# Kernel tuning notes

Hardware: AMD Instinct MI355X
Metric: run time of the kernel (lower is better)

Reference implementation:

```python
import jax, jax.numpy as jnp
import numpy as np

B, S, DIM = 4, 2048, 512
HEADS, DHEAD = 8, 64
INNER = HEADS * DHEAD


def setup_inputs() -> dict:
    key = jax.random.key(0)
    k1, k2, k3, k4 = jax.random.split(key, 4)
    x = jax.random.normal(k1, (B, S, DIM), dtype=jnp.float32)
    W_qkv = jax.random.normal(k2, (DIM, 3 * INNER), dtype=jnp.float32) * (DIM ** -0.5)
    W_out = jax.random.normal(k3, (INNER, DIM), dtype=jnp.float32) * (INNER ** -0.5)
    b_out = jnp.zeros((DIM,), dtype=jnp.float32)
    # learnable log-temperature, initialized to log(dim_head**-0.5)
    log_temp = jnp.asarray(np.log(DHEAD ** -0.5), dtype=jnp.float32)
    return {"x": x, "W_qkv": W_qkv, "log_temp": log_temp, "W_out": W_out, "b_out": b_out}


def reference(x, W_qkv, log_temp, W_out, b_out):
    b, s, _ = x.shape
    qkv = x @ W_qkv  # [b, s, 3*inner]
    q, k, v = jnp.split(qkv, 3, axis=-1)
    # [b, s, inner] -> [b, h, s, d]
    reshape = lambda t: t.reshape(b, s, HEADS, DHEAD).transpose(0, 2, 1, 3)
    q, k, v = reshape(q), reshape(k), reshape(v)
    dots = jnp.einsum("bhid,bhjd->bhij", q, k) * jnp.exp(log_temp)
    mask_value = -jnp.finfo(dots.dtype).max
    eye = jnp.eye(s, dtype=bool)
    dots = jnp.where(eye, mask_value, dots)
    attn = jax.nn.softmax(dots, axis=-1)
    out = jnp.einsum("bhij,bhjd->bhid", attn, v)
    out = out.transpose(0, 2, 1, 3).reshape(b, s, INNER)
    return out @ W_out + b_out
```

## Files before the change

### kernel.cpp

```cpp
#include <hip/hip_runtime.h>
#include <hip/hip_bf16.h>

#define BB 4
#define SS 2048
#define DIMM 512
#define HH 8
#define DD 64
#define NQKV 1536

typedef float  floatx4 __attribute__((ext_vector_type(4)));
typedef short  bf16x8  __attribute__((ext_vector_type(8)));
typedef short  bf16x4  __attribute__((ext_vector_type(4)));

#define MFMA16(A, B, C) __builtin_amdgcn_mfma_f32_16x16x32_bf16(A, B, C, 0, 0, 0)

__device__ __forceinline__ floatx4 MFMA16K16(bf16x4 a, bf16x4 b, floatx4 c) {
#if __has_builtin(__builtin_amdgcn_mfma_f32_16x16x16bf16_1k)
    return __builtin_amdgcn_mfma_f32_16x16x16bf16_1k(a, b, c, 0, 0, 0);
#else
    floatx4 d;
    asm volatile("v_mfma_f32_16x16x16_bf16 %0, %1, %2, %3"
                 : "=v"(d) : "v"(a), "v"(b), "v"(c));
    return d;
#endif
}

__device__ __forceinline__ unsigned short f2bf(float f) {
    unsigned int u = __float_as_uint(f);
    u += 0x7FFFu + ((u >> 16) & 1u);
    return (unsigned short)(u >> 16);
}

__device__ __forceinline__ unsigned int f2bf_pk(float lo, float hi) {
    float2 f; f.x = lo; f.y = hi;
    __hip_bfloat162 h = __float22bfloat162_rn(f);
    return *reinterpret_cast<unsigned int*>(&h);
}

__device__ __forceinline__ float fast_exp2(float x) {
#if __has_builtin(__builtin_amdgcn_exp2f)
    return __builtin_amdgcn_exp2f(x);
#else
    return __exp2f(x);
#endif
}

__device__ __forceinline__ void gl_lds16(const void* g, void* l) {
    __builtin_amdgcn_global_load_lds(
        (__attribute__((address_space(1))) void*)g,
        (__attribute__((address_space(3))) void*)l,
        16, 0, 0);
}

__global__ __launch_bounds__(256) void k_prep(
    const float* __restrict__ x, const float* __restrict__ W_qkv,
    const float* __restrict__ W_out,
    unsigned short* __restrict__ xb, unsigned short* __restrict__ Wq_t,
    unsigned short* __restrict__ Wo_t) {
    __shared__ float t[32][33];
    int bid = blockIdx.x, tid = threadIdx.x;
    if (bid < 4096) {
        int i = (bid * 256 + tid) * 4;
        float4 v = *(const float4*)(x + i);
        ushort4 o;
        o.x = f2bf(v.x); o.y = f2bf(v.y); o.z = f2bf(v.z); o.w = f2bf(v.w);
        *(ushort4*)(xb + i) = o;
        return;
    }
    const float* in; unsigned short* out; int R = 512, C, bx, by;
    if (bid < 4864) { in = W_qkv; out = Wq_t; C = 1536; int blk = bid - 4096; bx = blk % 48; by = blk / 48; }
    else            { in = W_out; out = Wo_t; C = 512;  int blk = bid - 4864; bx = blk % 16; by = blk / 16; }
    int tx = tid & 31, ty = tid >> 5;
    int c0 = bx * 32, r0 = by * 32;
    for (int i = 0; i < 4; i++) {
        int r = r0 + ty + i * 8;
        t[ty + i * 8][tx] = in[(size_t)r * C + c0 + tx];
    }
    __syncthreads();
    for (int i = 0; i < 4; i++) {
        int cc = c0 + ty + i * 8;
        out[(size_t)cc * R + r0 + tx] = f2bf(t[tx][ty + i * 8]);
    }
}

__global__ __launch_bounds__(256) void k_gemm_qkv(
    const unsigned short* __restrict__ A,
    const unsigned short* __restrict__ Bt,
    const float* __restrict__ log_temp,
    unsigned short* __restrict__ Qb,
    unsigned short* __restrict__ Kb,
    unsigned short* __restrict__ Vt) {
    __shared__ unsigned short smem[2][128 * 64];
    unsigned short* As = smem[0];
    unsigned short* Bs = smem[1];
    const int K = 512;
    int m0 = blockIdx.x * 128, n0 = blockIdx.y * 128;
    int tid = threadIdx.x;
    int w = tid >> 6, lane = tid & 63;
    int c = lane & 15, q4 = lane >> 4;
    int wm = w >> 1, wn = w & 1;
    float qscale = __expf(log_temp[0]) * 1.44269504f;

    floatx4 acc[4][4] = {};

    for (int k0 = 0; k0 < K; k0 += 64) {
        __syncthreads();
        for (int i = 0; i < 4; i++) {
            int cidx = w * 256 + i * 64 + lane;
            int row = cidx >> 3, cc = cidx & 7;
            int gcc = cc ^ (row & 7);
            gl_lds16(A + (size_t)(m0 + row) * K + k0 + gcc * 8,
                     As + (size_t)(w * 256 + i * 64) * 8);
            gl_lds16(Bt + (size_t)(n0 + row) * K + k0 + gcc * 8,
                     Bs + (size_t)(w * 256 + i * 64) * 8);
        }
        __syncthreads();
        bf16x8 aF[2][4], bF[2][4];
        for (int kh = 0; kh < 2; kh++)
            for (int mt = 0; mt < 4; mt++) {
                int row = wm * 64 + mt * 16 + c;
                aF[kh][mt] = *(const bf16x8*)&As[row * 64 + (((kh * 4 + q4) ^ (row & 7)) * 8)];
            }
        for (int kh = 0; kh < 2; kh++)
            for (int nt = 0; nt < 4; nt++) {
                int row = wn * 64 + nt * 16 + c;
                bF[kh][nt] = *(const bf16x8*)&Bs[row * 64 + (((kh * 4 + q4) ^ (row & 7)) * 8)];
            }
        for (int kh = 0; kh < 2; kh++)
            for (int mt = 0; mt < 4; mt++)
                for (int nt = 0; nt < 4; nt++)
                    acc[mt][nt] = MFMA16(aF[kh][mt], bF[kh][nt], acc[mt][nt]);
    }

    if (n0 < 1024) {
        for (int nt = 0; nt < 4; nt++) {
            int n = n0 + wn * 64 + nt * 16 + c;
            int t = n >> 9, inner = n & 511;
            int h = inner >> 6, d = inner & 63;
            for (int mt = 0; mt < 4; mt++) {
                for (int r = 0; r < 4; r++) {
                    int m = m0 + wm * 64 + mt * 16 + q4 * 4 + r;
                    int b = m >> 11, s = m & 2047;
                    int bh = b * 8 + h;
                    float v = acc[mt][nt][r];
                    if (t == 0)  Qb[((size_t)bh * SS + s) * 64 + d] = f2bf(v * qscale);
                    else         Kb[((size_t)bh * SS + s) * 64 + d] = f2bf(v);
                }
            }
        }
    } else {
        unsigned short* T = &smem[0][0];
        int b = m0 >> 11, s_base = m0 & 2047;
        for (int half = 0; half < 2; half++) {
            __syncthreads();
            if (wn == half) {
                for (int nt = 0; nt < 4; nt++)
                    for (int mt = 0; mt < 4; mt++)
                        for (int r = 0; r < 4; r++)
                            T[(nt * 16 + c) * 136 + wm * 64 + mt * 16 + q4 * 4 + r] =
                                f2bf(acc[mt][nt][r]);
            }
            __syncthreads();
            for (int rr = 0; rr < 4; rr++) {
                int nl = w * 16 + rr * 4 + q4;
                int ml = c * 8;
                bf16x8 v = *(const bf16x8*)&T[nl * 136 + ml];
                int n = n0 + half * 64 + nl;
                int h = (n >> 6) - 16, d = n & 63;
                int bh = b * 8 + h;
                *(bf16x8*)(Vt + ((size_t)bh * 64 + d) * SS + s_base + ml) = v;
            }
        }
    }
}

__global__ __launch_bounds__(512, 2) void k_attn(
    const unsigned short* __restrict__ Qb,
    const unsigned short* __restrict__ Kb,
    const unsigned short* __restrict__ Vt,
    unsigned short* __restrict__ AO) {
    __shared__ unsigned short Ks[2][64 * 64];
    __shared__ unsigned short Vs[2][64 * 64];
    int q0 = blockIdx.x * 256;
    int h = blockIdx.y, b = blockIdx.z;
    int bh = b * 8 + h;
    int tid = threadIdx.x, w = tid >> 6, lane = tid & 63;
    int c = lane & 15, q4 = lane >> 4;

    const unsigned short* Kbase = Kb + (size_t)bh * SS * 64;
    const unsigned short* Vbase = Vt + (size_t)bh * 64 * SS;

    bf16x8 qf[2][2];
    for (int mi = 0; mi < 2; mi++) {
        const unsigned short* qp = Qb + ((size_t)bh * SS + q0 + w * 32 + mi * 16 + c) * 64;
        qf[mi][0] = *(const bf16x8*)(qp + q4 * 8);
        qf[mi][1] = *(const bf16x8*)(qp + 32 + q4 * 8);
    }

    int grow = tid >> 3, gcc = (tid & 7) ^ (grow & 7);
    const unsigned short* ksrc = Kbase + (size_t)grow * 64 + gcc * 8;
    const unsigned short* vsrc = Vbase + (size_t)grow * SS + gcc * 8;
    unsigned short* kdst = (unsigned short*)Ks[0] + w * 512;
    unsigned short* vdst = (unsigned short*)Vs[0] + w * 512;

    gl_lds16(ksrc, kdst);
    gl_lds16(vsrc, vdst);

    int koff0 = (q4 ^ (c & 7)) * 8;
    int koff1 = ((4 + q4) ^ (c & 7)) * 8;
    int vsub = (q4 & 1) * 4;
    int vchunk0 = (q4 >> 1);

    int mask_j0 = (q0 + w * 32) & ~63;
    int mglob0 = q0 + w * 32 + c;
    int mglob1 = mglob0 + 16;
    floatx4 oacc[2][4] = {};
    float psum0 = 0.f, psum1 = 0.f;

    for (int j0 = 0; j0 < SS; j0 += 64) {
        int buf = (j0 >> 6) & 1;
        __syncthreads();
        if (j0 + 64 < SS) {
            gl_lds16(ksrc + (size_t)(j0 + 64) * 64, kdst + (buf ^ 1) * 4096);
            gl_lds16(vsrc + (j0 + 64), vdst + (buf ^ 1) * 4096);
        }
        bool diag = (j0 == mask_j0);
        const unsigned short* KsB = Ks[buf];
        const unsigned short* VsB = Vs[buf];

#pragma unroll
        for (int jt = 0; jt < 4; jt++) {
            int rowoff = (jt * 16 + c) * 64;
            bf16x8 kf0 = *(const bf16x8*)&KsB[rowoff + koff0];
            bf16x8 kf1 = *(const bf16x8*)&KsB[rowoff + koff1];
            floatx4 sa0 = {}, sa1 = {};
            sa0 = MFMA16(kf0, qf[0][0], sa0);
            sa0 = MFMA16(kf1, qf[0][1], sa0);
            sa1 = MFMA16(kf0, qf[1][0], sa1);
            sa1 = MFMA16(kf1, qf[1][1], sa1);

            if (diag) {
#pragma unroll
                for (int r = 0; r < 4; r++) {
                    int jg = j0 + jt * 16 + q4 * 4 + r;
                    if (jg == mglob0) sa0[r] = -1e30f;
                    if (jg == mglob1) sa1[r] = -1e30f;
                }
            }

            float e0 = fast_exp2(sa0[0]), e1 = fast_exp2(sa0[1]);
            float e2 = fast_exp2(sa0[2]), e3 = fast_exp2(sa0[3]);
            psum0 += (e0 + e1) + (e2 + e3);
            union { bf16x4 v; unsigned int u[2]; } P0;
            P0.u[0] = f2bf_pk(e0, e1); P0.u[1] = f2bf_pk(e2, e3);
            float f0 = fast_exp2(sa1[0]), f1 = fast_exp2(sa1[1]);
            float f2v = fast_exp2(sa1[2]), f3 = fast_exp2(sa1[3]);
            psum1 += (f0 + f1) + (f2v + f3);
            union { bf16x4 v; unsigned int u[2]; } P1;
            P1.u[0] = f2bf_pk(f0, f1); P1.u[1] = f2bf_pk(f2v, f3);

            int chunk = jt * 2 + vchunk0;
#pragma unroll
            for (int dt = 0; dt < 4; dt++) {
                int vrow = dt * 16 + c;
                bf16x4 vf = *(const bf16x4*)&VsB[vrow * 64 + ((chunk ^ (c & 7)) * 8) + vsub];
                oacc[0][dt] = MFMA16K16(P0.v, vf, oacc[0][dt]);
                oacc[1][dt] = MFMA16K16(P1.v, vf, oacc[1][dt]);
            }
        }
    }

    for (int mi = 0; mi < 2; mi++) {
        float l = (mi == 0) ? psum0 : psum1;
        l += __shfl_xor(l, 16);
        l += __shfl_xor(l, 32);
        for (int r = 0; r < 4; r++) {
            float lr = __shfl(l, q4 * 4 + r, 64);
            float inv = 1.0f / lr;
            int s = q0 + w * 32 + mi * 16 + q4 * 4 + r;
            for (int dt = 0; dt < 4; dt++)
                AO[((size_t)b * SS + s) * 512 + h * 64 + dt * 16 + c] =
                    f2bf(oacc[mi][dt][r] * inv);
        }
    }
}

__global__ __launch_bounds__(256) void k_gemm_out(
    const unsigned short* __restrict__ A,
    const unsigned short* __restrict__ Bt,
    const float* __restrict__ bias,
    float* __restrict__ out) {
    __shared__ unsigned short As[64 * 64];
    __shared__ unsigned short Bs[128 * 64];
    const int K = 512;
    int m0 = blockIdx.x * 64, n0 = blockIdx.y * 128;
    int tid = threadIdx.x;
    int w = tid >> 6, lane = tid & 63;
    int c = lane & 15, q4 = lane >> 4;

    floatx4 acc[8] = {};

    for (int k0 = 0; k0 < K; k0 += 64) {
        __syncthreads();
        for (int i = 0; i < 2; i++) {
            int cidx = i * 256 + tid;
            int row = cidx >> 3, cc = cidx & 7;
            int gcc = cc ^ (row & 7);
            gl_lds16(A + (size_t)(m0 + row) * K + k0 + gcc * 8,
                     As + (size_t)(i * 256 + w * 64) * 8);
        }
        for (int i = 0; i < 4; i++) {
            int cidx = i * 256 + tid;
            int row = cidx >> 3, cc = cidx & 7;
            int gcc = cc ^ (row & 7);
            gl_lds16(Bt + (size_t)(n0 + row) * K + k0 + gcc * 8,
                     Bs + (size_t)(i * 256 + w * 64) * 8);
        }
        __syncthreads();
        bf16x8 aF[2], bF[2][8];
        for (int kh = 0; kh < 2; kh++) {
            int row = w * 16 + c;
            aF[kh] = *(const bf16x8*)&As[row * 64 + (((kh * 4 + q4) ^ (row & 7)) * 8)];
        }
        for (int kh = 0; kh < 2; kh++)
            for (int nt = 0; nt < 8; nt++) {
                int row = nt * 16 + c;
                bF[kh][nt] = *(const bf16x8*)&Bs[row * 64 + (((kh * 4 + q4) ^ (row & 7)) * 8)];
            }
        for (int kh = 0; kh < 2; kh++)
            for (int nt = 0; nt < 8; nt++)
                acc[nt] = MFMA16(aF[kh], bF[kh][nt], acc[nt]);
    }

    for (int nt = 0; nt < 8; nt++) {
        int n = n0 + nt * 16 + c;
        float bv = bias[n];
        for (int r = 0; r < 4; r++) {
            int m = m0 + w * 16 + q4 * 4 + r;
            out[(size_t)m * 512 + n] = acc[nt][r] + bv;
        }
    }
}

extern "C" void kernel_launch(void* const* d_in, const int* in_sizes, int n_in,
                              void* d_out, int out_size, void* d_ws, size_t ws_size,
                              hipStream_t stream) {
    const float* x        = (const float*)d_in[0];
    const float* W_qkv    = (const float*)d_in[1];
    const float* log_temp = (const float*)d_in[2];
    const float* W_out    = (const float*)d_in[3];
    const float* b_out    = (const float*)d_in[4];
    float* out = (float*)d_out;

    char* ws = (char*)d_ws;
    unsigned short* xb   = (unsigned short*)(ws + 0);
    unsigned short* Wq_t = (unsigned short*)(ws + 8388608);
    unsigned short* Wo_t = (unsigned short*)(ws + 9961472);
    unsigned short* Qb   = (unsigned short*)(ws + 10485760);
    unsigned short* Kb   = (unsigned short*)(ws + 18874368);
    unsigned short* Vt   = (unsigned short*)(ws + 27262976);
    unsigned short* AO   = (unsigned short*)(ws + 35651584);

    k_prep<<<5120, 256, 0, stream>>>(x, W_qkv, W_out, xb, Wq_t, Wo_t);
    k_gemm_qkv<<<dim3(64, 12), 256, 0, stream>>>(xb, Wq_t, log_temp, Qb, Kb, Vt);
    k_attn<<<dim3(8, 8, 4), 512, 0, stream>>>(Qb, Kb, Vt, AO);
    k_gemm_out<<<dim3(128, 4), 256, 0, stream>>>(AO, Wo_t, b_out, out);
}
```

Baseline: 168.2 us.

## Triple-buffer K/V tiles in attention and halve block size to 256 threads

The attention kernel now uses 256-thread blocks covering 128 queries each, launching twice as many blocks. K/V tiles are triple-buffered and prefetched two tiles ahead, and the per-iteration __syncthreads is replaced by an explicit vmcnt wait plus s_barrier. The aim is to hide global-to-LDS latency behind the MFMA work and to raise occupancy and block count. In exchange each thread issues more loads, LDS use grows by half, and correctness now depends on the hand-counted vmcnt value.

```diff
diff --git a/kernel.cpp b/kernel.cpp
--- a/kernel.cpp
+++ b/kernel.cpp
@@ -174,14 +174,14 @@
     }
 }
 
-__global__ __launch_bounds__(512, 2) void k_attn(
+__global__ __launch_bounds__(256, 2) void k_attn(
     const unsigned short* __restrict__ Qb,
     const unsigned short* __restrict__ Kb,
     const unsigned short* __restrict__ Vt,
     unsigned short* __restrict__ AO) {
-    __shared__ unsigned short Ks[2][64 * 64];
-    __shared__ unsigned short Vs[2][64 * 64];
-    int q0 = blockIdx.x * 256;
+    __shared__ unsigned short Ks[3][64 * 64];
+    __shared__ unsigned short Vs[3][64 * 64];
+    int q0 = blockIdx.x * 128;
     int h = blockIdx.y, b = blockIdx.z;
     int bh = b * 8 + h;
     int tid = threadIdx.x, w = tid >> 6, lane = tid & 63;
@@ -197,14 +197,25 @@
         qf[mi][1] = *(const bf16x8*)(qp + 32 + q4 * 8);
     }
 
-    int grow = tid >> 3, gcc = (tid & 7) ^ (grow & 7);
-    const unsigned short* ksrc = Kbase + (size_t)grow * 64 + gcc * 8;
-    const unsigned short* vsrc = Vbase + (size_t)grow * SS + gcc * 8;
-    unsigned short* kdst = (unsigned short*)Ks[0] + w * 512;
-    unsigned short* vdst = (unsigned short*)Vs[0] + w * 512;
-
-    gl_lds16(ksrc, kdst);
-    gl_lds16(vsrc, vdst);
+    const unsigned short* ksrc[2];
+    const unsigned short* vsrc[2];
+    int ldst[2];
+    for (int i = 0; i < 2; i++) {
+        int cidx = i * 256 + tid;
+        int grow = cidx >> 3, gcc = (cidx & 7) ^ (grow & 7);
+        ksrc[i] = Kbase + (size_t)grow * 64 + gcc * 8;
+        vsrc[i] = Vbase + (size_t)grow * SS + gcc * 8;
+        ldst[i] = (i * 256 + w * 64) * 8;
+    }
+
+    for (int i = 0; i < 2; i++) {
+        gl_lds16(ksrc[i], &Ks[0][ldst[i]]);
+        gl_lds16(vsrc[i], &Vs[0][ldst[i]]);
+    }
+    for (int i = 0; i < 2; i++) {
+        gl_lds16(ksrc[i] + (size_t)64 * 64, &Ks[1][ldst[i]]);
+        gl_lds16(vsrc[i] + 64, &Vs[1][ldst[i]]);
+    }
 
     int koff0 = (q4 ^ (c & 7)) * 8;
     int koff1 = ((4 + q4) ^ (c & 7)) * 8;
@@ -217,13 +228,24 @@
     floatx4 oacc[2][4] = {};
     float psum0 = 0.f, psum1 = 0.f;
 
+    int buf = 0;
     for (int j0 = 0; j0 < SS; j0 += 64) {
-        int buf = (j0 >> 6) & 1;
-        __syncthreads();
         if (j0 + 64 < SS) {
-            gl_lds16(ksrc + (size_t)(j0 + 64) * 64, kdst + (buf ^ 1) * 4096);
-            gl_lds16(vsrc + (j0 + 64), vdst + (buf ^ 1) * 4096);
-        }
+            asm volatile("s_waitcnt vmcnt(4)" ::: "memory");
+        } else {
+            asm volatile("s_waitcnt vmcnt(0)" ::: "memory");
+        }
+        asm volatile("s_barrier" ::: "memory");
+
+        int jn = j0 + 128;
+        if (jn < SS) {
+            int bufn = buf + 2; if (bufn >= 3) bufn -= 3;
+            for (int i = 0; i < 2; i++) {
+                gl_lds16(ksrc[i] + (size_t)jn * 64, &Ks[bufn][ldst[i]]);
+                gl_lds16(vsrc[i] + jn, &Vs[bufn][ldst[i]]);
+            }
+        }
+
         bool diag = (j0 == mask_j0);
         const unsigned short* KsB = Ks[buf];
         const unsigned short* VsB = Vs[buf];
@@ -268,6 +290,7 @@
                 oacc[1][dt] = MFMA16K16(P1.v, vf, oacc[1][dt]);
             }
         }
+        buf = buf + 1; if (buf >= 3) buf = 0;
     }
 
     for (int mi = 0; mi < 2; mi++) {
@@ -363,6 +386,6 @@
 
     k_prep<<<5120, 256, 0, stream>>>(x, W_qkv, W_out, xb, Wq_t, Wo_t);
     k_gemm_qkv<<<dim3(64, 12), 256, 0, stream>>>(xb, Wq_t, log_temp, Qb, Kb, Vt);
-    k_attn<<<dim3(8, 8, 4), 512, 0, stream>>>(Qb, Kb, Vt, AO);
+    k_attn<<<dim3(16, 8, 4), 256, 0, stream>>>(Qb, Kb, Vt, AO);
     k_gemm_out<<<dim3(128, 4), 256, 0, stream>>>(AO, Wo_t, b_out, out);
 }
```

New measurement: 168.5 us. About the same (+0.2%).

## Stage 512-key K/V tiles in LDS and coalesce Q/K/V projection stores

Applied to the files above, without the earlier changes.

The QKV projection epilogue now writes Q and K through an LDS transpose buffer, giving vectorized coalesced row stores instead of scattered scalar stores. V^T is stored with a permuted column order so the attention kernel can load 8-element V fragments in one wide LDS read. The attention kernel drops the per-64-key double buffer and loads 512-key K/V chunks into a much larger LDS buffer, with one sync pair per chunk, and launch bounds change to one block per CU. This trades fewer barriers and wider LDS reads for lower occupancy and no overlap between loads and compute.

```diff
diff --git a/kernel.cpp b/kernel.cpp
--- a/kernel.cpp
+++ b/kernel.cpp
@@ -132,25 +132,34 @@
                     acc[mt][nt] = MFMA16(aF[kh][mt], bF[kh][nt], acc[mt][nt]);
     }
 
+    int b = m0 >> 11, s_base = m0 & 2047;
     if (n0 < 1024) {
-        for (int nt = 0; nt < 4; nt++) {
-            int n = n0 + wn * 64 + nt * 16 + c;
-            int t = n >> 9, inner = n & 511;
-            int h = inner >> 6, d = inner & 63;
-            for (int mt = 0; mt < 4; mt++) {
-                for (int r = 0; r < 4; r++) {
-                    int m = m0 + wm * 64 + mt * 16 + q4 * 4 + r;
-                    int b = m >> 11, s = m & 2047;
-                    int bh = b * 8 + h;
-                    float v = acc[mt][nt][r];
-                    if (t == 0)  Qb[((size_t)bh * SS + s) * 64 + d] = f2bf(v * qscale);
-                    else         Kb[((size_t)bh * SS + s) * 64 + d] = f2bf(v);
-                }
+        bool isQ = (n0 < 512);
+        float scale = isQ ? qscale : 1.0f;
+        unsigned short* dst = isQ ? Qb : Kb;
+        unsigned short* T = &smem[0][0];
+        for (int half = 0; half < 2; half++) {
+            __syncthreads();
+            if (wn == half) {
+                for (int nt = 0; nt < 4; nt++)
+                    for (int mt = 0; mt < 4; mt++)
+                        for (int r = 0; r < 4; r++)
+                            T[(wm * 64 + mt * 16 + q4 * 4 + r) * 72 + nt * 16 + c] =
+                                f2bf(acc[mt][nt][r] * scale);
+            }
+            __syncthreads();
+            int n_base = n0 + half * 64;
+            int hq = (n_base >> 6) & 7;
+            int bh = b * 8 + hq;
+            int gg = tid & 7;
+            for (int rr = 0; rr < 4; rr++) {
+                int m = (tid >> 3) + 32 * rr;
+                bf16x8 v = *(const bf16x8*)&T[m * 72 + gg * 8];
+                *(bf16x8*)(dst + ((size_t)bh * SS + s_base + m) * 64 + gg * 8) = v;
             }
         }
     } else {
         unsigned short* T = &smem[0][0];
-        int b = m0 >> 11, s_base = m0 & 2047;
         for (int half = 0; half < 2; half++) {
             __syncthreads();
             if (wn == half) {
@@ -168,19 +177,25 @@
                 int n = n0 + half * 64 + nl;
                 int h = (n >> 6) - 16, d = n & 63;
                 int bh = b * 8 + h;
-                *(bf16x8*)(Vt + ((size_t)bh * 64 + d) * SS + s_base + ml) = v;
-            }
-        }
-    }
-}
-
-__global__ __launch_bounds__(512, 2) void k_attn(
+                int wlo = ml >> 6, a = ml & 63;
+                int j1 = wlo * 64 + (((a >> 2) & 3) << 4) + ((a >> 4) << 2);
+                unsigned short* dp = Vt + ((size_t)bh * 64 + d) * SS + s_base + j1;
+                bf16x4 lo, hi;
+                for (int i = 0; i < 4; i++) { lo[i] = v[i]; hi[i] = v[4 + i]; }
+                *(bf16x4*)dp = lo;
+                *(bf16x4*)(dp + 16) = hi;
+            }
+        }
+    }
+}
+
+__global__ __launch_bounds__(512, 1) void k_attn(
     const unsigned short* __restrict__ Qb,
     const unsigned short* __restrict__ Kb,
     const unsigned short* __restrict__ Vt,
     unsigned short* __restrict__ AO) {
-    __shared__ unsigned short Ks[2][64 * 64];
-    __shared__ unsigned short Vs[2][64 * 64];
+    __shared__ unsigned short Ks[512 * 64];
+    __shared__ unsigned short Vs[64 * 512];
     int q0 = blockIdx.x * 256;
     int h = blockIdx.y, b = blockIdx.z;
     int bh = b * 8 + h;
@@ -197,19 +212,17 @@
         qf[mi][1] = *(const bf16x8*)(qp + 32 + q4 * 8);
     }
 
-    int grow = tid >> 3, gcc = (tid & 7) ^ (grow & 7);
-    const unsigned short* ksrc = Kbase + (size_t)grow * 64 + gcc * 8;
-    const unsigned short* vsrc = Vbase + (size_t)grow * SS + gcc * 8;
-    unsigned short* kdst = (unsigned short*)Ks[0] + w * 512;
-    unsigned short* vdst = (unsigned short*)Vs[0] + w * 512;
-
-    gl_lds16(ksrc, kdst);
-    gl_lds16(vsrc, vdst);
+    int r0 = tid >> 3;
+    const unsigned short* kstage = Kbase + (size_t)r0 * 64 + (((tid & 7) ^ (r0 & 7)) * 8);
+    const unsigned short* vstage = Vbase + (size_t)w * SS + (((tid >> 3) & 7) * 64)
+                                   + (((tid & 7) ^ w) * 8);
+    unsigned short* kdst = Ks + tid * 8;
+    unsigned short* vdst = Vs + tid * 8;
 
     int koff0 = (q4 ^ (c & 7)) * 8;
     int koff1 = ((4 + q4) ^ (c & 7)) * 8;
-    int vsub = (q4 & 1) * 4;
-    int vchunk0 = (q4 >> 1);
+    int voffA = ((2 * q4) ^ (c & 7)) * 8;
+    int voffB = ((2 * q4 + 1) ^ (c & 7)) * 8;
 
     int mask_j0 = (q0 + w * 32) & ~63;
     int mglob0 = q0 + w * 32 + c;
@@ -217,55 +230,70 @@
     floatx4 oacc[2][4] = {};
     float psum0 = 0.f, psum1 = 0.f;
 
-    for (int j0 = 0; j0 < SS; j0 += 64) {
-        int buf = (j0 >> 6) & 1;
-        __syncthreads();
-        if (j0 + 64 < SS) {
-            gl_lds16(ksrc + (size_t)(j0 + 64) * 64, kdst + (buf ^ 1) * 4096);
-            gl_lds16(vsrc + (j0 + 64), vdst + (buf ^ 1) * 4096);
-        }
-        bool diag = (j0 == mask_j0);
-        const unsigned short* KsB = Ks[buf];
-        const unsigned short* VsB = Vs[buf];
-
-#pragma unroll
-        for (int jt = 0; jt < 4; jt++) {
-            int rowoff = (jt * 16 + c) * 64;
-            bf16x8 kf0 = *(const bf16x8*)&KsB[rowoff + koff0];
-            bf16x8 kf1 = *(const bf16x8*)&KsB[rowoff + koff1];
-            floatx4 sa0 = {}, sa1 = {};
-            sa0 = MFMA16(kf0, qf[0][0], sa0);
-            sa0 = MFMA16(kf1, qf[0][1], sa0);
-            sa1 = MFMA16(kf0, qf[1][0], sa1);
-            sa1 = MFMA16(kf1, qf[1][1], sa1);
-
-            if (diag) {
-#pragma unroll
-                for (int r = 0; r < 4; r++) {
-                    int jg = j0 + jt * 16 + q4 * 4 + r;
-                    if (jg == mglob0) sa0[r] = -1e30f;
-                    if (jg == mglob1) sa1[r] = -1e30f;
-                }
-            }
-
-            float e0 = fast_exp2(sa0[0]), e1 = fast_exp2(sa0[1]);
-            float e2 = fast_exp2(sa0[2]), e3 = fast_exp2(sa0[3]);
-            psum0 += (e0 + e1) + (e2 + e3);
-            union { bf16x4 v; unsigned int u[2]; } P0;
-            P0.u[0] = f2bf_pk(e0, e1); P0.u[1] = f2bf_pk(e2, e3);
-            float f0 = fast_exp2(sa1[0]), f1 = fast_exp2(sa1[1]);
-            float f2v = fast_exp2(sa1[2]), f3 = fast_exp2(sa1[3]);
-            psum1 += (f0 + f1) + (f2v + f3);
-            union { bf16x4 v; unsigned int u[2]; } P1;
-            P1.u[0] = f2bf_pk(f0, f1); P1.u[1] = f2bf_pk(f2v, f3);
-
-            int chunk = jt * 2 + vchunk0;
+    for (int mg = 0; mg < 4; mg++) {
+        int js = mg * 512;
+        __syncthreads();
+#pragma unroll
+        for (int t = 0; t < 8; t++) {
+            gl_lds16(kstage + (size_t)(js + t * 64) * 64, kdst + t * 4096);
+            gl_lds16(vstage + js + (size_t)t * 8 * SS, vdst + t * 4096);
+        }
+        __syncthreads();
+
+        for (int sub = 0; sub < 8; sub++) {
+            int j0 = js + sub * 64;
+            const unsigned short* KsB = Ks + (sub * 64) * 64;
+            const unsigned short* VsB = Vs + sub * 64;
+            bool diag = (j0 == mask_j0);
+
+            bf16x8 vA[4], vB[4];
 #pragma unroll
             for (int dt = 0; dt < 4; dt++) {
                 int vrow = dt * 16 + c;
-                bf16x4 vf = *(const bf16x4*)&VsB[vrow * 64 + ((chunk ^ (c & 7)) * 8) + vsub];
-                oacc[0][dt] = MFMA16K16(P0.v, vf, oacc[0][dt]);
-                oacc[1][dt] = MFMA16K16(P1.v, vf, oacc[1][dt]);
+                vA[dt] = *(const bf16x8*)&VsB[vrow * 512 + voffA];
+                vB[dt] = *(const bf16x8*)&VsB[vrow * 512 + voffB];
+            }
+
+#pragma unroll
+            for (int jt = 0; jt < 4; jt++) {
+                int rowoff = (jt * 16 + c) * 64;
+                bf16x8 kf0 = *(const bf16x8*)&KsB[rowoff + koff0];
+                bf16x8 kf1 = *(const bf16x8*)&KsB[rowoff + koff1];
+                floatx4 sa0 = {}, sa1 = {};
+                sa0 = MFMA16(kf0, qf[0][0], sa0);
+                sa0 = MFMA16(kf1, qf[0][1], sa0);
+                sa1 = MFMA16(kf0, qf[1][0], sa1);
+                sa1 = MFMA16(kf1, qf[1][1], sa1);
+
+                if (diag) {
+#pragma unroll
+                    for (int r = 0; r < 4; r++) {
+                        int jg = j0 + jt * 16 + q4 * 4 + r;
+                        if (jg == mglob0) sa0[r] = -1e30f;
+                        if (jg == mglob1) sa1[r] = -1e30f;
+                    }
+                }
+
+                float e0 = fast_exp2(sa0[0]), e1 = fast_exp2(sa0[1]);
+                float e2 = fast_exp2(sa0[2]), e3 = fast_exp2(sa0[3]);
+                psum0 += (e0 + e1) + (e2 + e3);
+                union { bf16x4 v; unsigned int u[2]; } P0;
+                P0.u[0] = f2bf_pk(e0, e1); P0.u[1] = f2bf_pk(e2, e3);
+                float f0 = fast_exp2(sa1[0]), f1 = fast_exp2(sa1[1]);
+                float f2v = fast_exp2(sa1[2]), f3 = fast_exp2(sa1[3]);
+                psum1 += (f0 + f1) + (f2v + f3);
+                union { bf16x4 v; unsigned int u[2]; } P1;
+                P1.u[0] = f2bf_pk(f0, f1); P1.u[1] = f2bf_pk(f2v, f3);
+
+#pragma unroll
+                for (int dt = 0; dt < 4; dt++) {
+                    bf16x8 src = (jt < 2) ? vA[dt] : vB[dt];
+                    int s4 = (jt & 1) * 4;
+                    bf16x4 vf;
+                    for (int i = 0; i < 4; i++) vf[i] = src[s4 + i];
+                    oacc[0][dt] = MFMA16K16(P0.v, vf, oacc[0][dt]);
+                    oacc[1][dt] = MFMA16K16(P1.v, vf, oacc[1][dt]);
+                }
             }
         }
     }
```

Measured after the change: 169.7 us. No clear change (+0.9%).
